# Performance work log

Measured on AMD Instinct MI355X. Metric: run time of the kernel, lower is better.

## Reference

```python
import jax, jax.numpy as jnp
import numpy as np
import math

FACTOR = 3.0

def setup_inputs() -> dict:
    key = jax.random.key(0)
    k1, k2, k3 = jax.random.split(key, 3)
    B, L, H, E = 16, 4096, 8, 64
    queries = jax.random.normal(k1, (B, L, H, E), dtype=jnp.float32)
    keys = jax.random.normal(k2, (B, L, H, E), dtype=jnp.float32)
    values = jax.random.normal(k3, (B, L, H, E), dtype=jnp.float32)
    return {"queries": queries, "keys": keys, "values": values}

def reference(queries, keys, values):
    B, L, H, E = queries.shape
    top_k = int(FACTOR * math.log(L))  # 24 for L=4096 (static)
    # [B,H,E,L] layout for FFT along time
    q = jnp.transpose(queries, (0, 2, 3, 1))
    k = jnp.transpose(keys, (0, 2, 3, 1))
    v = jnp.transpose(values, (0, 2, 3, 1))
    # period-based autocorrelation via FFT cross-correlation
    qf = jnp.fft.rfft(q, axis=-1)
    kf = jnp.fft.rfft(k, axis=-1)
    corr = jnp.fft.irfft(qf * jnp.conj(kf), n=L, axis=-1)  # [B,H,E,L]
    # training-mode aggregation: shared top-k delay indices across batch
    mean_value = corr.mean(axis=(1, 2))                # [B,L]
    _, index = jax.lax.top_k(mean_value.mean(axis=0), top_k)  # [top_k]
    weights = mean_value[:, index]                     # [B,top_k]
    tmp_corr = jax.nn.softmax(weights, axis=-1)        # [B,top_k]
    delays_agg = jnp.zeros_like(v)
    for i in range(top_k):  # small static loop over delays
        pattern = jnp.roll(v, -index[i], axis=-1)
        delays_agg = delays_agg + pattern * tmp_corr[:, i][:, None, None, None]
    V = jnp.transpose(delays_agg, (0, 3, 1, 2))        # [B,L,H,E]
    return V
```

## Files before the change

### kernel.cpp

```cpp
#include <hip/hip_runtime.h>
#include <math.h>

#define B_ 16
#define L_ 4096
#define H_ 8
#define E_ 64
#define C_ 512
#define K_ 24
#define NT 256
#define RPAD 257

__device__ __forceinline__ float2 cmul(float2 a, float2 b) {
    return make_float2(a.x * b.x - a.y * b.y, a.x * b.y + a.y * b.x);
}
__device__ __forceinline__ float2 cadd(float2 a, float2 b) { return make_float2(a.x + b.x, a.y + b.y); }
__device__ __forceinline__ float2 csub(float2 a, float2 b) { return make_float2(a.x - b.x, a.y - b.y); }

__device__ __forceinline__ void bar_lds() {
    asm volatile("s_waitcnt lgkmcnt(0)" ::: "memory");
    __builtin_amdgcn_s_barrier();
}

__device__ __forceinline__ void fft16(float2 a[16]) {
    const float r2 = 0.70710678118654752f;
    const float c1 = 0.92387953251128676f;
    const float s1 = 0.38268343236508977f;
    const float2 W16[8] = {
        make_float2(1.f, 0.f),  make_float2(c1, -s1),  make_float2(r2, -r2),  make_float2(s1, -c1),
        make_float2(0.f, -1.f), make_float2(-s1, -c1), make_float2(-r2, -r2), make_float2(-c1, -s1)};
    #pragma unroll
    for (int j = 0; j < 8; ++j) {
        float2 u = a[j], v = a[j + 8];
        a[j]     = cadd(u, v);
        a[j + 8] = cmul(csub(u, v), W16[j]);
    }
    #pragma unroll
    for (int b = 0; b < 16; b += 8)
        #pragma unroll
        for (int j = 0; j < 4; ++j) {
            float2 u = a[b + j], v = a[b + j + 4];
            a[b + j]     = cadd(u, v);
            a[b + j + 4] = cmul(csub(u, v), W16[2 * j]);
        }
    #pragma unroll
    for (int b = 0; b < 16; b += 4)
        #pragma unroll
        for (int j = 0; j < 2; ++j) {
            float2 u = a[b + j], v = a[b + j + 2];
            a[b + j]     = cadd(u, v);
            a[b + j + 2] = cmul(csub(u, v), W16[4 * j]);
        }
    #pragma unroll
    for (int b = 0; b < 16; b += 2) {
        float2 u = a[b], v = a[b + 1];
        a[b]     = cadd(u, v);
        a[b + 1] = csub(u, v);
    }
}

__global__ __launch_bounds__(256) void k_zero(float* __restrict__ p, int n) {
    int i = blockIdx.x * 256 + threadIdx.x;
    if (i < n) p[i] = 0.f;
}

__global__ __launch_bounds__(256) void k_phaseA(const float* __restrict__ q,
                                                const float* __restrict__ k,
                                                float2* __restrict__ z,
                                                int b0) {
    __shared__ float2 s2[256 * 17];
    const int br4[16] = {0, 8, 4, 12, 2, 10, 6, 14, 1, 9, 5, 13, 3, 11, 7, 15};
    int w  = blockIdx.x;
    int g  = blockIdx.y;
    int bl = blockIdx.z;
    int b  = b0 + bl;
    int tid = threadIdx.x;

    const size_t base = (size_t)b * L_ * C_ + g * 16;
    int lrow = tid >> 2;
    int lq   = tid & 3;
    #pragma unroll
    for (int it = 0; it < 4; ++it) {
        int r   = lrow + (it << 6);
        int tau = ((r >> 4) << 8) + (w << 4) + (r & 15);
        const float4 q4 = *(const float4*)(q + base + (size_t)tau * C_ + (lq << 2));
        const float4 k4 = *(const float4*)(k + base + (size_t)tau * C_ + (lq << 2));
        float2* dst = &s2[r * 17 + (lq << 2)];
        dst[0] = make_float2(q4.x, k4.x);
        dst[1] = make_float2(q4.y, k4.y);
        dst[2] = make_float2(q4.z, k4.z);
        dst[3] = make_float2(q4.w, k4.w);
    }
    __syncthreads();

    int ch = tid >> 4, n2loc = tid & 15;
    int n2 = (w << 4) + n2loc;
    float2 a[16];
    int rbase = n2loc * 17 + ch;
    #pragma unroll
    for (int n1 = 0; n1 < 16; ++n1) a[n1] = s2[n1 * 272 + rbase];
    fft16(a);
    float sn, cs;
    sincospif((float)n2 / 2048.0f, &sn, &cs);
    const float2 w1 = make_float2(cs, -sn);
    float2 tw = w1;
    float2* zc = z + ((size_t)bl * C_ + (g * 16 + ch)) * L_ + n2;
    zc[0] = a[0];
    #pragma unroll
    for (int k1 = 1; k1 < 16; ++k1) {
        zc[(size_t)(k1 << 8)] = cmul(a[br4[k1]], tw);
        tw = cmul(tw, w1);
    }
}

__global__ __launch_bounds__(256) void k_fft_bc(const float2* __restrict__ z,
                                                float* __restrict__ cross,
                                                int b0) {
    __shared__ float2 s[16 * RPAD];
    __shared__ float2 tw256[256];
    const int br4[16] = {0, 8, 4, 12, 2, 10, 6, 14, 1, 9, 5, 13, 3, 11, 7, 15};
    int t  = threadIdx.x;
    int bl = blockIdx.y;
    int b  = b0 + bl;
    int c0 = blockIdx.x * 8;

    {
        int r1 = t >> 4, m2 = t & 15;
        float sn, cs;
        sincospif((float)(r1 * m2) / 128.0f, &sn, &cs);
        tw256[t] = make_float2(cs, -sn);
    }
    float accx[16], accy[16];
    #pragma unroll
    for (int r = 0; r < 16; ++r) { accx[r] = 0.f; accy[r] = 0.f; }

    const int rowB = t >> 4, m2B = t & 15;
    const int k1C = t & 15, r1C = t >> 4;

    float2 a[16];
    {
        const float2* zc0 = z + ((size_t)bl * C_ + c0) * L_;
        #pragma unroll
        for (int m1 = 0; m1 < 16; ++m1) a[m1] = zc0[(rowB << 8) + (m1 << 4) + m2B];
    }
    bar_lds();

    for (int cc = 0; cc < 8; ++cc) {
        fft16(a);
        #pragma unroll
        for (int r1 = 0; r1 < 16; ++r1)
            s[rowB * RPAD + (r1 << 4) + m2B] = cmul(a[br4[r1]], tw256[(r1 << 4) + m2B]);
        __syncthreads();
        #pragma unroll
        for (int m2 = 0; m2 < 16; ++m2) a[m2] = s[k1C * RPAD + (r1C << 4) + m2];
        fft16(a);
        __syncthreads();
        #pragma unroll
        for (int r2 = 0; r2 < 16; ++r2)
            s[(r2 << 8) + (r1C << 4) + k1C] = a[br4[r2]];
        if (cc < 7) {
            const float2* zn = z + ((size_t)bl * C_ + (c0 + cc + 1)) * L_;
            #pragma unroll
            for (int m1 = 0; m1 < 16; ++m1) a[m1] = zn[(rowB << 8) + (m1 << 4) + m2B];
        }
        bar_lds();
        #pragma unroll
        for (int r = 0; r < 16; ++r) {
            int p  = t + (r << 8);
            int pp = (L_ - p) & (L_ - 1);
            float2 A  = s[p];
            float2 Bv = s[pp];
            float Qr = 0.5f * (A.x + Bv.x);
            float Qi = 0.5f * (A.y - Bv.y);
            float Kr = 0.5f * (A.y + Bv.y);
            float Ki = 0.5f * (A.x - Bv.x);
            accx[r] += Qr * Kr - Qi * Ki;
            accy[r] += Qr * Ki + Qi * Kr;
        }
        bar_lds();
    }
    #pragma unroll
    for (int r = 0; r < 16; ++r) {
        int p = t + (r << 8);
        atomicAdd(&cross[((size_t)b * L_ + p) * 2 + 0], accx[r]);
        atomicAdd(&cross[((size_t)b * L_ + p) * 2 + 1], accy[r]);
    }
}

__global__ __launch_bounds__(256) void k_ifft(const float* __restrict__ cross,
                                              float* __restrict__ mv) {
    __shared__ float2 s[16 * RPAD];
    __shared__ float2 tw256[256];
    const int br4[16] = {0, 8, 4, 12, 2, 10, 6, 14, 1, 9, 5, 13, 3, 11, 7, 15};
    int t = threadIdx.x;
    int b = blockIdx.x;
    {
        int r1 = t >> 4, m2 = t & 15;
        float sn, cs;
        sincospif((float)(r1 * m2) / 128.0f, &sn, &cs);
        tw256[t] = make_float2(cs, -sn);
    }
    const float2* cr = (const float2*)cross + (size_t)b * L_;
    float2 a[16];
    #pragma unroll
    for (int n1 = 0; n1 < 16; ++n1) {
        float2 v = cr[(n1 << 8) + t];
        a[n1] = make_float2(v.x, -v.y);
    }
    fft16(a);
    {
        float sn, cs;
        sincospif((float)t / 2048.0f, &sn, &cs);
        const float2 w1 = make_float2(cs, -sn);
        float2 tw = w1;
        s[t] = a[0];
        #pragma unroll
        for (int k1 = 1; k1 < 16; ++k1) {
            s[k1 * RPAD + t] = cmul(a[br4[k1]], tw);
            tw = cmul(tw, w1);
        }
    }
    __syncthreads();
    const int rowB = t >> 4, m2B = t & 15;
    #pragma unroll
    for (int m1 = 0; m1 < 16; ++m1) a[m1] = s[rowB * RPAD + (m1 << 4) + m2B];
    fft16(a);
    #pragma unroll
    for (int r1 = 0; r1 < 16; ++r1)
        s[rowB * RPAD + (r1 << 4) + m2B] = cmul(a[br4[r1]], tw256[(r1 << 4) + m2B]);
    __syncthreads();
    const int k1C = t & 15, r1C = t >> 4;
    #pragma unroll
    for (int m2 = 0; m2 < 16; ++m2) a[m2] = s[k1C * RPAD + (r1C << 4) + m2];
    fft16(a);
    const float scale = 1.0f / ((float)L_ * (float)C_);
    #pragma unroll
    for (int r2 = 0; r2 < 16; ++r2)
        mv[(size_t)b * L_ + (r2 << 8) + t] = a[br4[r2]].x * scale;
}

__global__ __launch_bounds__(256) void k_topk(const float* __restrict__ mv,
                                              int* __restrict__ idx,
                                              float* __restrict__ wts) {
    __shared__ float wv[4];
    __shared__ int   wi[4];
    __shared__ int   idxL[K_];
    int tid = threadIdx.x;
    float vloc[16];
    #pragma unroll
    for (int r = 0; r < 16; ++r) {
        int tt = tid + (r << 8);
        float ssum = 0.f;
        for (int b = 0; b < B_; ++b) ssum += mv[(size_t)b * L_ + tt];
        vloc[r] = ssum;
    }
    int lane = tid & 63, w = tid >> 6;
    for (int i = 0; i < K_; ++i) {
        float best = -INFINITY; int bi = 1 << 30;
        #pragma unroll
        for (int r = 0; r < 16; ++r) {
            float v = vloc[r]; int ii = tid + (r << 8);
            if (v > best || (v == best && ii < bi)) { best = v; bi = ii; }
        }
        #pragma unroll
        for (int off = 32; off > 0; off >>= 1) {
            float ov = __shfl_down(best, off);
            int   oi = __shfl_down(bi, off);
            if (ov > best || (ov == best && oi < bi)) { best = ov; bi = oi; }
        }
        if (lane == 0) { wv[w] = best; wi[w] = bi; }
        __syncthreads();
        if (tid == 0) {
            float bb = wv[0]; int bj = wi[0];
            for (int j = 1; j < 4; ++j)
                if (wv[j] > bb || (wv[j] == bb && wi[j] < bj)) { bb = wv[j]; bj = wi[j]; }
            idxL[i] = bj; idx[i] = bj;
        }
        __syncthreads();
        int win = idxL[i];
        #pragma unroll
        for (int r = 0; r < 16; ++r)
            if (win == tid + (r << 8)) vloc[r] = -INFINITY;
    }
    if (tid < B_) {
        int b = tid;
        float ww[K_]; float wm = -INFINITY;
        for (int i = 0; i < K_; ++i) { ww[i] = mv[(size_t)b * L_ + idxL[i]]; wm = fmaxf(wm, ww[i]); }
        float ssum = 0.f;
        for (int i = 0; i < K_; ++i) { ww[i] = expf(ww[i] - wm); ssum += ww[i]; }
        float inv = 1.f / ssum;
        for (int i = 0; i < K_; ++i) wts[b * K_ + i] = ww[i] * inv;
    }
}

__global__ __launch_bounds__(256) void k_agg(const float* __restrict__ vals,
                                             const int* __restrict__ idx,
                                             const float* __restrict__ wts,
                                             float* __restrict__ out) {
    __shared__ float4 sv[L_];
    __shared__ int   di[K_];
    __shared__ float dw[K_];
    const int tid = threadIdx.x;
    int id = blockIdx.x;
    int wk = ((id & 7) << 8) | (id >> 3);
    int b  = wk >> 7;
    int c0 = (wk & 127) << 2;

    if (tid < K_) { di[tid] = idx[tid]; dw[tid] = wts[b * K_ + tid]; }

    const float* gbase = vals + (size_t)b * L_ * C_ + c0;
    #pragma unroll
    for (int it = 0; it < 16; ++it) {
        int tau = (it << 8) + tid;
        const float* g = gbase + (size_t)tau * C_;
        float4* l = &sv[(it << 8) + ((tid >> 6) << 6)];
        __builtin_amdgcn_global_load_lds(
            (const __attribute__((address_space(1))) uint32_t*)g,
            (__attribute__((address_space(3))) uint32_t*)l,
            16, 0, 0);
    }
    __syncthreads();

    int   dir[K_]; float dwr[K_];
    #pragma unroll
    for (int i = 0; i < K_; ++i) { dir[i] = di[i]; dwr[i] = dw[i]; }

    float* obase = out + (size_t)b * L_ * C_ + c0;
    for (int r = 0; r < 16; ++r) {
        int tau = (r << 8) + tid;
        float4 acc = make_float4(0.f, 0.f, 0.f, 0.f);
        #pragma unroll
        for (int i = 0; i < K_; ++i) {
            float4 x = sv[(tau + dir[i]) & (L_ - 1)];
            float w = dwr[i];
            acc.x = fmaf(w, x.x, acc.x);
            acc.y = fmaf(w, x.y, acc.y);
            acc.z = fmaf(w, x.z, acc.z);
            acc.w = fmaf(w, x.w, acc.w);
        }
        *(float4*)(obase + (size_t)tau * C_) = acc;
    }
}

extern "C" void kernel_launch(void* const* d_in, const int* in_sizes, int n_in,
                              void* d_out, int out_size, void* d_ws, size_t ws_size,
                              hipStream_t stream) {
    const float* q = (const float*)d_in[0];
    const float* k = (const float*)d_in[1];
    const float* v = (const float*)d_in[2];
    float* out = (float*)d_out;
    char* ws = (char*)d_ws;

    float* cross = (float*)ws;
    float* mv    = (float*)(ws + (1 << 20));
    int*   idx   = (int*)(ws + (1 << 20) + (1 << 18));
    float* wts   = (float*)(ws + (1 << 20) + (1 << 18) + 4096);
    float2* z    = (float2*)(ws + (2 << 20));

    size_t zcap = (ws_size > (size_t)(2 << 20)) ? ws_size - (size_t)(2 << 20) : 0;
    int P = 16;
    while (P > 1 && (size_t)P * C_ * L_ * sizeof(float2) > zcap) P >>= 1;

    k_zero<<<(B_ * L_ * 2 + 255) / 256, 256, 0, stream>>>(cross, B_ * L_ * 2);

    for (int b0 = 0; b0 < B_; b0 += P) {
        dim3 g1(16, 32, P);
        k_phaseA<<<g1, 256, 0, stream>>>(q, k, z, b0);
        dim3 g2(C_ / 8, P);
        k_fft_bc<<<g2, 256, 0, stream>>>(z, cross, b0);
    }
    k_ifft<<<B_, 256, 0, stream>>>(cross, mv);
    k_topk<<<1, 256, 0, stream>>>(mv, idx, wts);
    k_agg<<<B_ * (C_ / 4) / 8 * 8, 256, 0, stream>>>(v, idx, wts, out);
}
```

Baseline: 361.1 us.

## Fuse first FFT pass into full per-channel FFT kernel, dropping intermediate z buffer

Replaces the two-kernel scheme (phaseA writing a 4096-point intermediate z to global memory, then fft_bc finishing the FFT) with one 1024-thread kernel. Each block loads q/k columns for 4 channels, runs the full 4096-point FFT in LDS per 256-thread group, and processes two channel sets per block. It also reduces the four groups' cross-spectra in LDS before the atomics, which cuts atomic traffic. This removes a large global write and read of z but raises LDS use and block size, which may lower occupancy.

```diff
diff --git a/kernel.cpp b/kernel.cpp
--- a/kernel.cpp
+++ b/kernel.cpp
@@ -9,6 +9,7 @@
 #define K_ 24
 #define NT 256
 #define RPAD 257
+#define WSZ 4112
 
 __device__ __forceinline__ float2 cmul(float2 a, float2 b) {
     return make_float2(a.x * b.x - a.y * b.y, a.x * b.y + a.y * b.x);
@@ -63,112 +64,112 @@
     if (i < n) p[i] = 0.f;
 }
 
-__global__ __launch_bounds__(256) void k_phaseA(const float* __restrict__ q,
-                                                const float* __restrict__ k,
-                                                float2* __restrict__ z,
-                                                int b0) {
-    __shared__ float2 s2[256 * 17];
-    const int br4[16] = {0, 8, 4, 12, 2, 10, 6, 14, 1, 9, 5, 13, 3, 11, 7, 15};
-    int w  = blockIdx.x;
-    int g  = blockIdx.y;
-    int bl = blockIdx.z;
-    int b  = b0 + bl;
-    int tid = threadIdx.x;
-
-    const size_t base = (size_t)b * L_ * C_ + g * 16;
-    int lrow = tid >> 2;
-    int lq   = tid & 3;
-    #pragma unroll
-    for (int it = 0; it < 4; ++it) {
-        int r   = lrow + (it << 6);
-        int tau = ((r >> 4) << 8) + (w << 4) + (r & 15);
-        const float4 q4 = *(const float4*)(q + base + (size_t)tau * C_ + (lq << 2));
-        const float4 k4 = *(const float4*)(k + base + (size_t)tau * C_ + (lq << 2));
-        float2* dst = &s2[r * 17 + (lq << 2)];
-        dst[0] = make_float2(q4.x, k4.x);
-        dst[1] = make_float2(q4.y, k4.y);
-        dst[2] = make_float2(q4.z, k4.z);
-        dst[3] = make_float2(q4.w, k4.w);
-    }
-    __syncthreads();
-
-    int ch = tid >> 4, n2loc = tid & 15;
-    int n2 = (w << 4) + n2loc;
-    float2 a[16];
-    int rbase = n2loc * 17 + ch;
-    #pragma unroll
-    for (int n1 = 0; n1 < 16; ++n1) a[n1] = s2[n1 * 272 + rbase];
-    fft16(a);
-    float sn, cs;
-    sincospif((float)n2 / 2048.0f, &sn, &cs);
-    const float2 w1 = make_float2(cs, -sn);
-    float2 tw = w1;
-    float2* zc = z + ((size_t)bl * C_ + (g * 16 + ch)) * L_ + n2;
-    zc[0] = a[0];
-    #pragma unroll
-    for (int k1 = 1; k1 < 16; ++k1) {
-        zc[(size_t)(k1 << 8)] = cmul(a[br4[k1]], tw);
-        tw = cmul(tw, w1);
-    }
-}
-
-__global__ __launch_bounds__(256) void k_fft_bc(const float2* __restrict__ z,
-                                                float* __restrict__ cross,
-                                                int b0) {
-    __shared__ float2 s[16 * RPAD];
+__global__ __launch_bounds__(1024) void k_fft_full(const float* __restrict__ q,
+                                                   const float* __restrict__ k,
+                                                   float* __restrict__ cross) {
+    __shared__ float2 w4[4 * WSZ];
     __shared__ float2 tw256[256];
     const int br4[16] = {0, 8, 4, 12, 2, 10, 6, 14, 1, 9, 5, 13, 3, 11, 7, 15};
-    int t  = threadIdx.x;
-    int bl = blockIdx.y;
-    int b  = b0 + bl;
-    int c0 = blockIdx.x * 8;
-
-    {
-        int r1 = t >> 4, m2 = t & 15;
+    const int tid = threadIdx.x;
+    const int t   = tid & 255;
+    const int grp = tid >> 8;
+
+    int id = blockIdx.x;
+    int wk = ((id & 7) << 7) | (id >> 3);
+    int b  = wk >> 6;
+    int g  = wk & 63;
+
+    if (tid < 256) {
+        int r1 = tid >> 4, m2 = tid & 15;
         float sn, cs;
         sincospif((float)(r1 * m2) / 128.0f, &sn, &cs);
-        tw256[t] = make_float2(cs, -sn);
-    }
-    float accx[16], accy[16];
-    #pragma unroll
-    for (int r = 0; r < 16; ++r) { accx[r] = 0.f; accy[r] = 0.f; }
+        tw256[tid] = make_float2(cs, -sn);
+    }
 
     const int rowB = t >> 4, m2B = t & 15;
     const int k1C = t & 15, r1C = t >> 4;
-
-    float2 a[16];
+    const int sw3 = (tid >> 3) & 3;
+    const int chx = grp ^ sw3;
+
+    float accx[16], accy[16];
+    #pragma unroll
+    for (int r = 0; r < 16; ++r) { accx[r] = 0.f; accy[r] = 0.f; }
+
+    float snA, csA;
+    sincospif((float)t / 2048.0f, &snA, &csA);
+    const float2 w1 = make_float2(csA, -snA);
+
+    const size_t rowbase = (size_t)b * L_ * C_;
+    float4 qr[4], kr[4];
     {
-        const float2* zc0 = z + ((size_t)bl * C_ + c0) * L_;
-        #pragma unroll
-        for (int m1 = 0; m1 < 16; ++m1) a[m1] = zc0[(rowB << 8) + (m1 << 4) + m2B];
-    }
-    bar_lds();
-
-    for (int cc = 0; cc < 8; ++cc) {
+        int cb = g << 2;
+        #pragma unroll
+        for (int it = 0; it < 4; ++it) {
+            int tau = (it << 10) + tid;
+            qr[it] = *(const float4*)(q + rowbase + (size_t)tau * C_ + cb);
+            kr[it] = *(const float4*)(k + rowbase + (size_t)tau * C_ + cb);
+        }
+    }
+
+    float2* wg = w4 + grp * WSZ;
+
+    for (int rnd = 0; rnd < 2; ++rnd) {
+        #pragma unroll
+        for (int it = 0; it < 4; ++it) {
+            int tau = (it << 10) + tid;
+            float2* row = w4 + (tau << 2);
+            row[0 ^ sw3] = make_float2(qr[it].x, kr[it].x);
+            row[1 ^ sw3] = make_float2(qr[it].y, kr[it].y);
+            row[2 ^ sw3] = make_float2(qr[it].z, kr[it].z);
+            row[3 ^ sw3] = make_float2(qr[it].w, kr[it].w);
+        }
+        __syncthreads();
+        float2 a[16];
+        #pragma unroll
+        for (int n1 = 0; n1 < 16; ++n1)
+            a[n1] = w4[(((n1 << 8) + t) << 2) + chx];
+        bar_lds();
         fft16(a);
+        {
+            float2 tw = w1;
+            wg[t] = a[0];
+            #pragma unroll
+            for (int k1 = 1; k1 < 16; ++k1) {
+                wg[k1 * RPAD + t] = cmul(a[br4[k1]], tw);
+                tw = cmul(tw, w1);
+            }
+        }
+        __syncthreads();
+        #pragma unroll
+        for (int m1 = 0; m1 < 16; ++m1) a[m1] = wg[rowB * RPAD + (m1 << 4) + m2B];
+        fft16(a);
         #pragma unroll
         for (int r1 = 0; r1 < 16; ++r1)
-            s[rowB * RPAD + (r1 << 4) + m2B] = cmul(a[br4[r1]], tw256[(r1 << 4) + m2B]);
-        __syncthreads();
-        #pragma unroll
-        for (int m2 = 0; m2 < 16; ++m2) a[m2] = s[k1C * RPAD + (r1C << 4) + m2];
+            wg[rowB * RPAD + (r1 << 4) + m2B] = cmul(a[br4[r1]], tw256[(r1 << 4) + m2B]);
+        __syncthreads();
+        #pragma unroll
+        for (int m2 = 0; m2 < 16; ++m2) a[m2] = wg[k1C * RPAD + (r1C << 4) + m2];
         fft16(a);
         __syncthreads();
         #pragma unroll
         for (int r2 = 0; r2 < 16; ++r2)
-            s[(r2 << 8) + (r1C << 4) + k1C] = a[br4[r2]];
-        if (cc < 7) {
-            const float2* zn = z + ((size_t)bl * C_ + (c0 + cc + 1)) * L_;
+            wg[(r2 << 8) + (r1C << 4) + k1C] = a[br4[r2]];
+        if (rnd == 0) {
+            int cb = (g << 2) + 256;
             #pragma unroll
-            for (int m1 = 0; m1 < 16; ++m1) a[m1] = zn[(rowB << 8) + (m1 << 4) + m2B];
+            for (int it = 0; it < 4; ++it) {
+                int tau = (it << 10) + tid;
+                qr[it] = *(const float4*)(q + rowbase + (size_t)tau * C_ + cb);
+                kr[it] = *(const float4*)(k + rowbase + (size_t)tau * C_ + cb);
+            }
         }
         bar_lds();
         #pragma unroll
         for (int r = 0; r < 16; ++r) {
             int p  = t + (r << 8);
             int pp = (L_ - p) & (L_ - 1);
-            float2 A  = s[p];
-            float2 Bv = s[pp];
+            float2 A  = wg[p];
+            float2 Bv = wg[pp];
             float Qr = 0.5f * (A.x + Bv.x);
             float Qi = 0.5f * (A.y - Bv.y);
             float Kr = 0.5f * (A.y + Bv.y);
@@ -178,11 +179,24 @@
         }
         bar_lds();
     }
-    #pragma unroll
-    for (int r = 0; r < 16; ++r) {
-        int p = t + (r << 8);
-        atomicAdd(&cross[((size_t)b * L_ + p) * 2 + 0], accx[r]);
-        atomicAdd(&cross[((size_t)b * L_ + p) * 2 + 1], accy[r]);
+
+    #pragma unroll
+    for (int r = 0; r < 16; ++r)
+        wg[t * 16 + (r ^ (t & 15))] = make_float2(accx[r], accy[r]);
+    __syncthreads();
+    float* crb = cross + (size_t)b * L_ * 2;
+    #pragma unroll
+    for (int rr = 0; rr < 4; ++rr) {
+        int p  = tid + (rr << 10);
+        int tl = p & 255, rv = p >> 8;
+        float sx = 0.f, sy = 0.f;
+        #pragma unroll
+        for (int gg = 0; gg < 4; ++gg) {
+            float2 vv = w4[gg * WSZ + tl * 16 + (rv ^ (tl & 15))];
+            sx += vv.x; sy += vv.y;
+        }
+        atomicAdd(&crb[p * 2 + 0], sx);
+        atomicAdd(&crb[p * 2 + 1], sy);
     }
 }
 
@@ -354,21 +368,10 @@
     float* mv    = (float*)(ws + (1 << 20));
     int*   idx   = (int*)(ws + (1 << 20) + (1 << 18));
     float* wts   = (float*)(ws + (1 << 20) + (1 << 18) + 4096);
-    float2* z    = (float2*)(ws + (2 << 20));
-
-    size_t zcap = (ws_size > (size_t)(2 << 20)) ? ws_size - (size_t)(2 << 20) : 0;
-    int P = 16;
-    while (P > 1 && (size_t)P * C_ * L_ * sizeof(float2) > zcap) P >>= 1;
 
     k_zero<<<(B_ * L_ * 2 + 255) / 256, 256, 0, stream>>>(cross, B_ * L_ * 2);
-
-    for (int b0 = 0; b0 < B_; b0 += P) {
-        dim3 g1(16, 32, P);
-        k_phaseA<<<g1, 256, 0, stream>>>(q, k, z, b0);
-        dim3 g2(C_ / 8, P);
-        k_fft_bc<<<g2, 256, 0, stream>>>(z, cross, b0);
-    }
+    k_fft_full<<<B_ * (C_ / 8), 1024, 0, stream>>>(q, k, cross);
     k_ifft<<<B_, 256, 0, stream>>>(cross, mv);
     k_topk<<<1, 256, 0, stream>>>(mv, idx, wts);
-    k_agg<<<B_ * (C_ / 4) / 8 * 8, 256, 0, stream>>>(v, idx, wts, out);
-}
+    k_agg<<<B_ * (C_ / 4), 256, 0, stream>>>(v, idx, wts, out);
+}
```

Measured after the change: 675.0 us. 1.87x slower.

## Replace atomic cross-spectrum accumulation with Hermitian-half partials and a reduction kernel

Applied to the files above, without the earlier changes.

The cross-power spectrum is Hermitian, so only bins 0..2048 are computed. Each block writes its partial sums to a per-group buffer instead of issuing global atomicAdds, and a new reduce kernel sums the 64 groups. The inverse FFT reads the upper half as conjugates, and the zero kernel is removed. The phaseA twiddle recurrence is split into four independent chains to shorten the dependent multiply sequence, at the cost of extra workspace and one more launch.

```diff
diff --git a/kernel.cpp b/kernel.cpp
--- a/kernel.cpp
+++ b/kernel.cpp
@@ -9,6 +9,8 @@
 #define K_ 24
 #define NT 256
 #define RPAD 257
+#define PSTRIDE 2052
+#define G_ 64
 
 __device__ __forceinline__ float2 cmul(float2 a, float2 b) {
     return make_float2(a.x * b.x - a.y * b.y, a.x * b.y + a.y * b.x);
@@ -56,11 +58,6 @@
         a[b]     = cadd(u, v);
         a[b + 1] = csub(u, v);
     }
-}
-
-__global__ __launch_bounds__(256) void k_zero(float* __restrict__ p, int n) {
-    int i = blockIdx.x * 256 + threadIdx.x;
-    if (i < n) p[i] = 0.f;
 }
 
 __global__ __launch_bounds__(256) void k_phaseA(const float* __restrict__ q,
@@ -102,18 +99,21 @@
     float sn, cs;
     sincospif((float)n2 / 2048.0f, &sn, &cs);
     const float2 w1 = make_float2(cs, -sn);
-    float2 tw = w1;
+    const float2 w2 = cmul(w1, w1);
+    const float2 w4 = cmul(w2, w2);
+    float2 tws[4] = {w1, w2, cmul(w2, w1), w4};
     float2* zc = z + ((size_t)bl * C_ + (g * 16 + ch)) * L_ + n2;
     zc[0] = a[0];
     #pragma unroll
     for (int k1 = 1; k1 < 16; ++k1) {
-        zc[(size_t)(k1 << 8)] = cmul(a[br4[k1]], tw);
-        tw = cmul(tw, w1);
+        int j = (k1 - 1) & 3;
+        zc[(size_t)(k1 << 8)] = cmul(a[br4[k1]], tws[j]);
+        tws[j] = cmul(tws[j], w4);
     }
 }
 
 __global__ __launch_bounds__(256) void k_fft_bc(const float2* __restrict__ z,
-                                                float* __restrict__ cross,
+                                                float2* __restrict__ part,
                                                 int b0) {
     __shared__ float2 s[16 * RPAD];
     __shared__ float2 tw256[256];
@@ -121,7 +121,8 @@
     int t  = threadIdx.x;
     int bl = blockIdx.y;
     int b  = b0 + bl;
-    int c0 = blockIdx.x * 8;
+    int g  = blockIdx.x;
+    int c0 = g * 8;
 
     {
         int r1 = t >> 4, m2 = t & 15;
@@ -129,9 +130,9 @@
         sincospif((float)(r1 * m2) / 128.0f, &sn, &cs);
         tw256[t] = make_float2(cs, -sn);
     }
-    float accx[16], accy[16];
-    #pragma unroll
-    for (int r = 0; r < 16; ++r) { accx[r] = 0.f; accy[r] = 0.f; }
+    float accx[8], accy[8], accN = 0.f;
+    #pragma unroll
+    for (int r = 0; r < 8; ++r) { accx[r] = 0.f; accy[r] = 0.f; }
 
     const int rowB = t >> 4, m2B = t & 15;
     const int k1C = t & 15, r1C = t >> 4;
@@ -164,7 +165,7 @@
         }
         bar_lds();
         #pragma unroll
-        for (int r = 0; r < 16; ++r) {
+        for (int r = 0; r < 8; ++r) {
             int p  = t + (r << 8);
             int pp = (L_ - p) & (L_ - 1);
             float2 A  = s[p];
@@ -176,13 +177,38 @@
             accx[r] += Qr * Kr - Qi * Ki;
             accy[r] += Qr * Ki + Qi * Kr;
         }
+        accN += s[2048].x * s[2048].y;
         bar_lds();
     }
-    #pragma unroll
-    for (int r = 0; r < 16; ++r) {
-        int p = t + (r << 8);
-        atomicAdd(&cross[((size_t)b * L_ + p) * 2 + 0], accx[r]);
-        atomicAdd(&cross[((size_t)b * L_ + p) * 2 + 1], accy[r]);
+    float2* pb = part + (size_t)(b * G_ + g) * PSTRIDE;
+    #pragma unroll
+    for (int r = 0; r < 8; ++r)
+        pb[t + (r << 8)] = make_float2(accx[r], accy[r]);
+    if (t == 0) pb[2048] = make_float2(accN, 0.f);
+}
+
+__global__ __launch_bounds__(256) void k_reduce(const float2* __restrict__ part,
+                                                float* __restrict__ cross) {
+    __shared__ float2 acc2[128];
+    int b  = blockIdx.x;
+    int pt = blockIdx.y;
+    int t  = threadIdx.x;
+    int pi = t & 127, gh = t >> 7;
+    int p  = pt * 128 + pi;
+    float sx = 0.f, sy = 0.f;
+    if (p <= 2048) {
+        const float2* base = part + ((size_t)b * G_ + gh * 32) * PSTRIDE + p;
+        #pragma unroll 4
+        for (int g = 0; g < 32; ++g) {
+            float2 v = base[(size_t)g * PSTRIDE];
+            sx += v.x; sy += v.y;
+        }
+    }
+    if (gh == 1) acc2[pi] = make_float2(sx, sy);
+    __syncthreads();
+    if (gh == 0 && p <= 2048) {
+        float2 o = acc2[pi];
+        ((float2*)cross)[(size_t)b * L_ + p] = make_float2(sx + o.x, sy + o.y);
     }
 }
 
@@ -203,8 +229,10 @@
     float2 a[16];
     #pragma unroll
     for (int n1 = 0; n1 < 16; ++n1) {
-        float2 v = cr[(n1 << 8) + t];
-        a[n1] = make_float2(v.x, -v.y);
+        int P = (n1 << 8) + t;
+        int hi = P > 2048;
+        float2 v = cr[hi ? (L_ - P) : P];
+        a[n1] = hi ? v : make_float2(v.x, -v.y);
     }
     fft16(a);
     {
@@ -350,25 +378,26 @@
     float* out = (float*)d_out;
     char* ws = (char*)d_ws;
 
-    float* cross = (float*)ws;
-    float* mv    = (float*)(ws + (1 << 20));
-    int*   idx   = (int*)(ws + (1 << 20) + (1 << 18));
-    float* wts   = (float*)(ws + (1 << 20) + (1 << 18) + 4096);
-    float2* z    = (float2*)(ws + (2 << 20));
-
-    size_t zcap = (ws_size > (size_t)(2 << 20)) ? ws_size - (size_t)(2 << 20) : 0;
+    float*  cross = (float*)ws;
+    float*  mv    = (float*)(ws + (1 << 20));
+    int*    idx   = (int*)(ws + (1 << 20) + (1 << 18));
+    float*  wts   = (float*)(ws + (1 << 20) + (1 << 18) + 4096);
+    float2* part  = (float2*)(ws + (2 << 20));
+    float2* z     = (float2*)(ws + (size_t)(20 << 20));
+
+    size_t zcap = (ws_size > (size_t)(20 << 20)) ? ws_size - (size_t)(20 << 20) : 0;
     int P = 16;
     while (P > 1 && (size_t)P * C_ * L_ * sizeof(float2) > zcap) P >>= 1;
-
-    k_zero<<<(B_ * L_ * 2 + 255) / 256, 256, 0, stream>>>(cross, B_ * L_ * 2);
 
     for (int b0 = 0; b0 < B_; b0 += P) {
         dim3 g1(16, 32, P);
         k_phaseA<<<g1, 256, 0, stream>>>(q, k, z, b0);
-        dim3 g2(C_ / 8, P);
-        k_fft_bc<<<g2, 256, 0, stream>>>(z, cross, b0);
-    }
+        dim3 g2(G_, P);
+        k_fft_bc<<<g2, 256, 0, stream>>>(z, part, b0);
+    }
+    dim3 gr(B_, 17);
+    k_reduce<<<gr, 256, 0, stream>>>(part, cross);
     k_ifft<<<B_, 256, 0, stream>>>(cross, mv);
     k_topk<<<1, 256, 0, stream>>>(mv, idx, wts);
-    k_agg<<<B_ * (C_ / 4) / 8 * 8, 256, 0, stream>>>(v, idx, wts, out);
-}
+    k_agg<<<B_ * (C_ / 4), 256, 0, stream>>>(v, idx, wts, out);
+}
```

Measured after the change: 329.2 us. 8.8% less time.
